# Kernel tuning notes

Hardware: AMD Instinct MI355X
Metric: run time of the kernel (lower is better)

## Reference

```python
import jax, jax.numpy as jnp
import numpy as np

NQ, NS, D, DC, HT = 100000, 2000, 128, 64, 128
B, T = 128, 500
NNZ_HG, NNZ_GCN, NNZ_SIM = 300000, 64000, 1000000
NUM_MV, NUM_QL = 2, 2


def spmm(rows, cols, vals, x, n_rows):
    # y = A @ x, A sparse COO with A[rows[k], cols[k]] = vals[k]
    return jax.ops.segment_sum(vals[:, None] * x[cols], rows, num_segments=n_rows)


def gcn_conv(x, src, dst, W, b, n):
    # PyG-style GCNConv: sym-normalized (A + I), then linear + bias
    h = x @ W
    loop = jnp.arange(n, dtype=src.dtype)
    s = jnp.concatenate([src, loop])
    d = jnp.concatenate([dst, loop])
    deg = jax.ops.segment_sum(jnp.ones(s.shape[0], jnp.float32), d, num_segments=n)
    dinv = jax.lax.rsqrt(jnp.maximum(deg, 1.0))
    norm = dinv[s] * dinv[d]
    return jax.ops.segment_sum(norm[:, None] * h[s], d, num_segments=n) + b


def setup_inputs() -> dict:
    key = jax.random.key(0)
    ks = iter(jax.random.split(key, 64))
    nrm = lambda shape, s=0.05: jax.random.normal(next(ks), shape, jnp.float32) * s
    ri = lambda shape, hi: jax.random.randint(next(ks), shape, 0, hi, jnp.int32)
    inp = {}
    inp['question_seq'] = ri((B, T), NQ)
    inp['skill_seq'] = ri((B, T), NS)
    inp['answer_seq'] = ri((B, T), 2)
    inp['hg_q'] = ri((NNZ_HG,), NQ)
    inp['hg_c'] = ri((NNZ_HG,), NS)
    inp['gcn_src'] = ri((NNZ_GCN,), NS)
    inp['gcn_dst'] = ri((NNZ_GCN,), NS)
    inp['sim_src'] = ri((NNZ_SIM,), NQ)
    inp['sim_dst'] = ri((NNZ_SIM,), NQ)
    inp['hg_vals_qc'] = jax.random.uniform(next(ks), (NNZ_HG,), jnp.float32) * 0.05
    inp['hg_vals_cq'] = jax.random.uniform(next(ks), (NNZ_HG,), jnp.float32) * 0.05
    inp['sim_vals'] = jax.random.uniform(next(ks), (NNZ_SIM,), jnp.float32) * 0.02
    inp['q_emb'] = nrm((NQ + 1, D))
    inp['s_emb'] = nrm((NS + 1, D))
    inp['c_emb'] = nrm((3, DC))
    for nm in ['w_g1', 'w_g2', 'w_g3']:
        inp[nm] = nrm((D, D))
    for nm in ['b_g1', 'b_g2', 'b_g3']:
        inp[nm] = nrm((1, D))
    for i in [1, 2, 3]:
        inp['gcn_w%d' % i] = nrm((D, D))
        inp['gcn_b%d' % i] = nrm((D,))
    for nm in ['w_sg1', 'w_sg2', 'w_qg1', 'w_qg3']:
        inp[nm] = nrm((D, 1))
    for nm in ['b_sg1', 'b_sg2', 'b_qg1', 'b_qg3']:
        inp[nm] = nrm((1,))
    LIN = 2 * D + DC
    inp['w_ih'] = nrm((4 * HT, LIN))
    inp['w_hh'] = nrm((4 * HT, HT))
    inp['b_ih'] = nrm((4 * HT,))
    inp['b_hh'] = nrm((4 * HT,))
    inp['fc1_w'] = nrm((HT + 2 * D, HT))
    inp['fc1_b'] = nrm((HT,))
    inp['fc2_w'] = nrm((HT, 1))
    inp['fc2_b'] = nrm((1,))
    return inp


def reference(question_seq, skill_seq, answer_seq, hg_q, hg_c, gcn_src, gcn_dst,
              sim_src, sim_dst, hg_vals_qc, hg_vals_cq, sim_vals,
              q_emb, s_emb, c_emb, w_g1, w_g2, w_g3, b_g1, b_g2, b_g3,
              gcn_w1, gcn_b1, gcn_w2, gcn_b2, gcn_w3, gcn_b3,
              w_sg1, w_sg2, w_qg1, w_qg3, b_sg1, b_sg2, b_qg1, b_qg3,
              w_ih, w_hh, b_ih, b_hh, fc1_w, fc1_b, fc2_w, fc2_b):
    sig = jax.nn.sigmoid
    # gated (channel-specific) embedding tables, excluding padding row
    one_gate = s_emb[:-1] * sig(s_emb[:-1] @ w_g1 + b_g1)
    two_gate = s_emb[:-1] * sig(s_emb[:-1] @ w_g2 + b_g2)
    three_gate = q_emb[:-1] * sig(q_emb[:-1] @ w_g3 + b_g3)

    # channel 1: multi-view hypergraph conv with residual + mean over layers (dropout p=0 -> identity)
    embs = [one_gate]
    x = one_gate
    for _ in range(NUM_MV):
        m = spmm(hg_q, hg_c, hg_vals_qc, x, NQ)   # HG_qc @ x -> [NQ, D]
        x = spmm(hg_c, hg_q, hg_vals_cq, m, NS)   # HG_cq @ m -> [NS, D]
        x = x + embs[-1]
        embs.append(x)
    one_skill = jnp.mean(jnp.stack(embs), 0)
    one_q = spmm(hg_q, hg_c, hg_vals_qc, one_skill, NQ)  # structural question embs
    one_skill_p = jnp.concatenate([one_skill, s_emb[-1:]], 0)
    one_q_p = jnp.concatenate([one_q, q_emb[-1:]], 0)
    one_b_skill = one_skill_p[skill_seq]   # [B,T,D]
    one_b_q = one_q_p[question_seq]        # [B,T,D]

    # channel 2: 3-layer GCN with relu (dropout p=0)
    x = jax.nn.relu(gcn_conv(two_gate, gcn_src, gcn_dst, gcn_w1, gcn_b1, NS))
    x = jax.nn.relu(gcn_conv(x, gcn_src, gcn_dst, gcn_w2, gcn_b2, NS))
    x = jax.nn.relu(gcn_conv(x, gcn_src, gcn_dst, gcn_w3, gcn_b3, NS))
    two_skill_p = jnp.concatenate([x, s_emb[-1:]], 0)
    two_b_skill = two_skill_p[skill_seq]

    # channel 3: question similarity conv with residual + mean over layers
    embs = [three_gate]
    x = three_gate
    for _ in range(NUM_QL):
        x = spmm(sim_src, sim_dst, sim_vals, x, NQ) + embs[-1]
        embs.append(x)
    three_q = jnp.mean(jnp.stack(embs), 0)
    three_q_p = jnp.concatenate([three_q, q_emb[-1:]], 0)
    three_b_q = three_q_p[question_seq]

    # gated channel fusion
    fused_skill = sig(one_b_skill @ w_sg1 + b_sg1) * one_b_skill \
                + sig(two_b_skill @ w_sg2 + b_sg2) * two_b_skill
    fused_q = sig(one_b_q @ w_qg1 + b_qg1) * one_b_q \
            + sig(three_b_q @ w_qg3 + b_qg3) * three_b_q
    corr = c_emb[answer_seq]  # [B,T,DC]
    lstm_in = jnp.concatenate([fused_q, fused_skill, corr], -1)  # [B,T,2D+DC]

    def step(carry, xt):
        h, c = carry
        z = xt @ w_ih.T + b_ih + h @ w_hh.T + b_hh
        i, f, g, o = jnp.split(z, 4, axis=-1)  # torch LSTM gate order
        c = sig(f) * c + sig(i) * jnp.tanh(g)
        h = sig(o) * jnp.tanh(c)
        return (h, c), h

    b = lstm_in.shape[0]
    h0 = jnp.zeros((b, HT), lstm_in.dtype)
    _, hs = jax.lax.scan(step, (h0, h0), jnp.swapaxes(lstm_in, 0, 1))
    hs = jnp.swapaxes(hs, 0, 1)  # [B,T,HT]

    pred_in = jnp.concatenate([hs, fused_q, fused_skill], -1)  # [B,T,HT+2D]
    preds = sig(jax.nn.relu(pred_in @ fc1_w + fc1_b) @ fc2_w + fc2_b)  # [B,T,1]
    return preds
```

## Files before the change

### kernel.cpp

```cpp
#include <hip/hip_runtime.h>

#define NQc 100000
#define NSc 2000
#define Dc 128
#define DCc 64
#define HTc 128
#define Bc 128
#define Tc 500
#define BTc (Bc*Tc)
#define NNZ_HGc 300000
#define NNZ_GCNc 64000
#define NNZ_SIMc 1000000
#define LINc 320
#define G4c 512

using bf16x8  = __attribute__((ext_vector_type(8))) short;
using floatx4 = __attribute__((ext_vector_type(4))) float;
typedef _Float16 half2v __attribute__((ext_vector_type(2)));

__device__ __forceinline__ float sigf(float x){ return 1.0f/(1.0f + __expf(-x)); }
__device__ __forceinline__ float tanhfast(float x){ return 2.0f*sigf(2.0f*x) - 1.0f; }

__device__ __forceinline__ unsigned short bf16r(float x){
  unsigned u = __float_as_uint(x);
  unsigned r = (u + 0x7FFFu + ((u>>16)&1u)) >> 16;
  return (unsigned short)r;
}
__device__ __forceinline__ unsigned pack2(float2 v){
  return (unsigned)bf16r(v.x) | ((unsigned)bf16r(v.y) << 16);
}
__device__ __forceinline__ float bflo(unsigned u){ return __uint_as_float(u << 16); }
__device__ __forceinline__ float bfhi(unsigned u){ return __uint_as_float(u & 0xFFFF0000u); }

__device__ __forceinline__ float wredsum(float v){
  #pragma unroll
  for (int off=32; off>0; off>>=1) v += __shfl_xor(v, off, 64);
  return v;
}

__global__ void fill_kernel(float* p, float v, int n){
  int i = blockIdx.x*blockDim.x + threadIdx.x;
  if (i<n) p[i] = v;
}

__global__ void cvt_bf16_kernel(const float* __restrict__ in, unsigned short* __restrict__ out, long n){
  long i = (long)blockIdx.x*blockDim.x + threadIdx.x;
  long stride = (long)gridDim.x*blockDim.x;
  for (; i<n; i+=stride) out[i] = bf16r(in[i]);
}

__global__ void cvt_weights_kernel(
    const float* __restrict__ w_ih, unsigned short* __restrict__ w_ih_bf,
    const float* __restrict__ fc1_w, unsigned short* __restrict__ fc1_wT,
    const float* __restrict__ w_g3, unsigned short* __restrict__ w_g3T,
    const float* __restrict__ w_hh, _Float16* __restrict__ w_hh_h,
    const float* __restrict__ b_ih, const float* __restrict__ b_hh, float* __restrict__ biasP)
{
  int i = blockIdx.x*blockDim.x + threadIdx.x;
  const int T0 = G4c*LINc;
  const int T1 = T0 + 384*HTc;
  const int T2 = T1 + Dc*Dc;
  const int T3 = T2 + G4c*HTc;
  const int T4 = T3 + G4c;
  if (i < T0){
    int r = i/LINc, c = i%LINc;
    int rp = (r&127)*4 + (r>>7);
    w_ih_bf[(size_t)rp*LINc + c] = bf16r(w_ih[i]);
  } else if (i < T1){
    int j = i - T0; int r = j/HTc, c = j%HTc;
    fc1_wT[(size_t)c*384 + r] = bf16r(fc1_w[j]);
  } else if (i < T2){
    int j = i - T1; int r = j/Dc, c = j%Dc;
    w_g3T[(size_t)c*Dc + r] = bf16r(w_g3[j]);
  } else if (i < T3){
    int j = i - T2;
    w_hh_h[j] = (_Float16)w_hh[j];
  } else if (i < T4){
    int j = i - T3;
    biasP[(j&127)*4 + (j>>7)] = b_ih[j] + b_hh[j];
  }
}

__global__ void hist_all_kernel(const int* __restrict__ sim_src, int* cnt_sim,
                                const int* __restrict__ hg_q, int* cnt_hgq,
                                const int* __restrict__ hg_c, int* cnt_hgc,
                                const int* __restrict__ gcn_dst, int* cnt_gcn){
  long i = (long)blockIdx.x*blockDim.x + threadIdx.x;
  long stride = (long)gridDim.x*blockDim.x;
  const long T0=NNZ_SIMc, T1=T0+NNZ_HGc, T2=T1+NNZ_HGc, T3=T2+NNZ_GCNc;
  for (; i<T3; i+=stride){
    if (i<T0)      atomicAdd(&cnt_sim[sim_src[i]], 1);
    else if (i<T1) atomicAdd(&cnt_hgq[hg_q[i-T0]], 1);
    else if (i<T2) atomicAdd(&cnt_hgc[hg_c[i-T1]], 1);
    else           atomicAdd(&cnt_gcn[gcn_dst[i-T2]], 1);
  }
}

#define BS_STRIDE 104
__global__ __launch_bounds__(1024) void scan_local_all_kernel(
    const int* __restrict__ cnt_sim, int* rp_sim,
    const int* __restrict__ cnt_hgq, int* rp_hgq,
    const int* __restrict__ cnt_hgc, int* rp_hgc,
    const int* __restrict__ cnt_gcn, int* rp_gcn,
    int* __restrict__ bsum, float* __restrict__ dinv)
{
  __shared__ int buf[1024];
  int b = blockIdx.x, tid = threadIdx.x;
  const int* cnt; int* rp; int* bs; int n; int lb; int seg;
  if (b < 98)      { seg=0; cnt=cnt_sim; rp=rp_sim; n=NQc; lb=b; }
  else if (b <196) { seg=1; cnt=cnt_hgq; rp=rp_hgq; n=NQc; lb=b-98; }
  else if (b <198) { seg=2; cnt=cnt_hgc; rp=rp_hgc; n=NSc; lb=b-196; }
  else             { seg=3; cnt=cnt_gcn; rp=rp_gcn; n=NSc; lb=b-198; }
  bs = bsum + seg*BS_STRIDE;
  int i = lb*1024 + tid;
  int v = (i<n) ? cnt[i] : 0;
  if (seg==3 && i<n) dinv[i] = rsqrtf((float)v + 1.0f);
  buf[tid] = v;
  __syncthreads();
  for (int off=1; off<1024; off<<=1){
    int t = (tid>=off) ? buf[tid-off] : 0;
    __syncthreads();
    buf[tid] += t;
    __syncthreads();
  }
  if (i<n) rp[i] = buf[tid] - v;
  if (tid==1023) bs[lb] = buf[1023];
}
__global__ __launch_bounds__(128) void scan_bsum_all_kernel(int* bsum){
  __shared__ int s[128];
  int seg = blockIdx.x, tid = threadIdx.x;
  int nb = (seg<2) ? 98 : 2;
  int* bs = bsum + seg*BS_STRIDE;
  int v = (tid<nb) ? bs[tid] : 0;
  s[tid] = v;
  __syncthreads();
  for (int off=1; off<128; off<<=1){
    int t = (tid>=off) ? s[tid-off] : 0;
    __syncthreads();
    s[tid] += t;
    __syncthreads();
  }
  if (tid<nb) bs[tid] = s[tid] - v;
  if (tid==0) bs[nb] = s[127];
}
__global__ void scan_add_all_kernel(
    int* rp_sim, int* cnt_sim, int* rp_hgq, int* cnt_hgq,
    int* rp_hgc, int* cnt_hgc, int* rp_gcn, int* cnt_gcn,
    const int* __restrict__ bsum)
{
  int b = blockIdx.x, tid = threadIdx.x;
  int* rp; int* cur; const int* bs; int n; int lb; int nb;
  if (b < 391)      { rp=rp_sim; cur=cnt_sim; bs=bsum;               n=NQc; lb=b;     nb=98; }
  else if (b < 782) { rp=rp_hgq; cur=cnt_hgq; bs=bsum+BS_STRIDE;     n=NQc; lb=b-391; nb=98; }
  else if (b < 790) { rp=rp_hgc; cur=cnt_hgc; bs=bsum+2*BS_STRIDE;   n=NSc; lb=b-782; nb=2; }
  else              { rp=rp_gcn; cur=cnt_gcn; bs=bsum+3*BS_STRIDE;   n=NSc; lb=b-790; nb=2; }
  int i = lb*256 + tid;
  if (i<n){ int r = rp[i] + bs[i>>10]; rp[i]=r; cur[i]=r; }
  if (lb==0 && tid==0) rp[n] = bs[nb];
}

__global__ void scatter_all_kernel(
    const int* __restrict__ sim_src, const int* __restrict__ sim_dst, const float* __restrict__ sim_vals,
    int* cur_sim, int* col_sim, float* val_sim,
    const int* __restrict__ hg_q, const int* __restrict__ hg_c,
    const float* __restrict__ hg_vals_qc, const float* __restrict__ hg_vals_cq,
    int* cur_hgq, int* col_hgq, float* val_hgq,
    int* cur_hgc, int* col_hgc, float* val_hgc,
    const int* __restrict__ gcn_dst, const int* __restrict__ gcn_src,
    int* cur_gcn, int* src_gcn)
{
  long i = (long)blockIdx.x*blockDim.x + threadIdx.x;
  long stride = (long)gridDim.x*blockDim.x;
  const long T0=NNZ_SIMc, T1=T0+NNZ_HGc, T2=T1+NNZ_HGc, T3=T2+NNZ_GCNc;
  for (; i<T3; i+=stride){
    if (i<T0){
      int r = sim_src[i]; int p = atomicAdd(&cur_sim[r],1);
      col_sim[p] = sim_dst[i]; val_sim[p] = sim_vals[i];
    } else if (i<T1){
      long j=i-T0; int r = hg_q[j]; int p = atomicAdd(&cur_hgq[r],1);
      col_hgq[p] = hg_c[j]; val_hgq[p] = hg_vals_qc[j];
    } else if (i<T2){
      long j=i-T1; int r = hg_c[j]; int p = atomicAdd(&cur_hgc[r],1);
      col_hgc[p] = hg_q[j]; val_hgc[p] = hg_vals_cq[j];
    } else {
      long j=i-T2; int r = gcn_dst[j]; int p = atomicAdd(&cur_gcn[r],1);
      src_gcn[p] = gcn_src[j];
    }
  }
}

#define BM 64
#define BN 64
#define BK 16
__global__ __launch_bounds__(256) void gemm_kernel(
    const float* __restrict__ A, int lda,
    const float* __restrict__ Bm, float* __restrict__ C,
    unsigned short* __restrict__ Cbf, float* __restrict__ Ccopy,
    const float* __restrict__ bias, const float* __restrict__ gsrc,
    int M, int N, int K, int ep)
{
  __shared__ float As[BM][BK+4];
  __shared__ float Bs[BK][BN+4];
  int tid = threadIdx.x;
  int tx = tid & 15, ty = tid >> 4;
  int mBase = blockIdx.y*BM, nBase = blockIdx.x*BN;
  float acc[4][4];
  #pragma unroll
  for (int i=0;i<4;i++)
    #pragma unroll
    for (int j=0;j<4;j++) acc[i][j]=0.f;
  int arow = tid>>2, ac4 = tid&3;
  for (int kt=0; kt<K; kt+=BK){
    {
      int m = mBase + arow;
      float4 v = make_float4(0.f,0.f,0.f,0.f);
      if (m < M) v = *(const float4*)(A + (size_t)m*lda + kt + ac4*4);
      *(float4*)&As[arow][ac4*4] = v;
    }
    {
      int kr = tid>>4, c4 = tid&15;
      float4 v = *(const float4*)(Bm + (size_t)(kt+kr)*N + nBase + c4*4);
      *(float4*)&Bs[kr][c4*4] = v;
    }
    __syncthreads();
    #pragma unroll
    for (int k=0;k<BK;k++){
      float a0=As[ty*4+0][k],a1=As[ty*4+1][k],a2=As[ty*4+2][k],a3=As[ty*4+3][k];
      float b0=Bs[k][tx*4+0],b1=Bs[k][tx*4+1],b2=Bs[k][tx*4+2],b3=Bs[k][tx*4+3];
      acc[0][0]+=a0*b0; acc[0][1]+=a0*b1; acc[0][2]+=a0*b2; acc[0][3]+=a0*b3;
      acc[1][0]+=a1*b0; acc[1][1]+=a1*b1; acc[1][2]+=a1*b2; acc[1][3]+=a1*b3;
      acc[2][0]+=a2*b0; acc[2][1]+=a2*b1; acc[2][2]+=a2*b2; acc[2][3]+=a2*b3;
      acc[3][0]+=a3*b0; acc[3][1]+=a3*b1; acc[3][2]+=a3*b2; acc[3][3]+=a3*b3;
    }
    __syncthreads();
  }
  #pragma unroll
  for (int i=0;i<4;i++){
    int m = mBase + ty*4 + i;
    if (m >= M) continue;
    #pragma unroll
    for (int j=0;j<4;j++){
      int n = nBase + tx*4 + j;
      float v = acc[i][j];
      if (bias)  v += bias[n];
      if (ep==1)      v = gsrc[(size_t)m*N + n] * sigf(v);
      C[(size_t)m*N + n] = v;
      if (Cbf)   Cbf[(size_t)m*N + n] = bf16r(v);
      if (Ccopy) Ccopy[(size_t)m*N + n] = v;
    }
  }
}

__global__ __launch_bounds__(256) void mfma_gemm_kernel(
    const unsigned short* __restrict__ A1, int lda1,
    const unsigned short* __restrict__ A2, int lda2, int ksplit,
    const unsigned short* __restrict__ Bt,
    float* __restrict__ C, unsigned short* __restrict__ Cbf,
    const float* __restrict__ bias, const float* __restrict__ bias2,
    const float* __restrict__ gsrc,
    const float* __restrict__ fc2w, const float* __restrict__ fc2b, float* __restrict__ outp,
    int M, int N, int K, int ep)
{
  __shared__ unsigned short Asm[128*64];
  __shared__ unsigned short Bsm[128*64];
  __shared__ float rps[2][128];
  int tid = threadIdx.x;
  int wave = tid>>6, lane = tid&63;
  int quad = lane>>4, l16 = lane&15;
  int m0 = blockIdx.y*128, n0 = blockIdx.x*128;
  int wm = (wave&1)*64, wn = (wave>>1)*64;
  floatx4 acc[4][4];
  #pragma unroll
  for (int i=0;i<4;i++)
    #pragma unroll
    for (int j=0;j<4;j++) acc[i][j] = (floatx4){0.f,0.f,0.f,0.f};

  for (int kt=0; kt<K; kt+=64){
    #pragma unroll
    for (int i=0;i<4;i++){
      int idx = i*256 + tid;
      int row = idx>>3, blk = idx&7;
      int kcol = kt + blk*8;
      {
        const unsigned short* src = (kcol < ksplit)
            ? (A1 + (size_t)(m0+row)*lda1 + kcol)
            : (A2 + (size_t)(m0+row)*lda2 + (kcol - ksplit));
        float4 v = *(const float4*)src;
        *(float4*)&Asm[row*64 + ((blk ^ (row&7))<<3)] = v;
      }
      {
        const unsigned short* src = Bt + (size_t)(n0+row)*K + kcol;
        float4 v = *(const float4*)src;
        *(float4*)&Bsm[row*64 + ((blk ^ (row&7))<<3)] = v;
      }
    }
    __syncthreads();
    #pragma unroll
    for (int ks=0; ks<2; ks++){
      bf16x8 af[4], bfr[4];
      #pragma unroll
      for (int mt=0;mt<4;mt++){
        int row = wm + mt*16 + l16;
        int blk = ks*4 + quad;
        af[mt] = *(const bf16x8*)&Asm[row*64 + ((blk ^ (row&7))<<3)];
      }
      #pragma unroll
      for (int nt=0;nt<4;nt++){
        int row = wn + nt*16 + l16;
        int blk = ks*4 + quad;
        bfr[nt] = *(const bf16x8*)&Bsm[row*64 + ((blk ^ (row&7))<<3)];
      }
      #pragma unroll
      for (int mt=0;mt<4;mt++)
        #pragma unroll
        for (int nt=0;nt<4;nt++)
          acc[mt][nt] = __builtin_amdgcn_mfma_f32_16x16x32_bf16(af[mt], bfr[nt], acc[mt][nt], 0,0,0);
    }
    __syncthreads();
  }
  if (ep == 3){
    float fw[4], fb[4];
    #pragma unroll
    for (int nt=0;nt<4;nt++){ int col = wn + nt*16 + l16; fw[nt] = fc2w[col]; fb[nt] = bias[col]; }
    #pragma unroll
    for (int mt=0;mt<4;mt++){
      #pragma unroll
      for (int r=0;r<4;r++){
        float s = 0.f;
        #pragma unroll
        for (int nt=0;nt<4;nt++){
          float v = acc[mt][nt][r] + fb[nt];
          v = fmaxf(v, 0.f);
          s += v*fw[nt];
        }
        s += __shfl_xor(s,1); s += __shfl_xor(s,2); s += __shfl_xor(s,4); s += __shfl_xor(s,8);
        if (l16 == 0) rps[wave>>1][wm + mt*16 + quad*4 + r] = s;
      }
    }
    __syncthreads();
    if (tid < 128){
      int row = m0 + tid;
      if (row < M) outp[row] = sigf(rps[0][tid] + rps[1][tid] + fc2b[0]);
    }
    return;
  }
  #pragma unroll
  for (int mt=0;mt<4;mt++){
    #pragma unroll
    for (int nt=0;nt<4;nt++){
      int col = n0 + wn + nt*16 + l16;
      #pragma unroll
      for (int r=0;r<4;r++){
        int row = m0 + wm + mt*16 + quad*4 + r;
        if (row < M){
          float v = acc[mt][nt][r];
          if (bias)  v += bias[col];
          if (bias2) v += bias2[col];
          if (ep==1)      v = gsrc[(size_t)row*N + col] * sigf(v);
          else if (ep==2) v = fmaxf(v, 0.f);
          C[(size_t)row*N + col] = v;
          if (Cbf) Cbf[(size_t)row*N + col] = bf16r(v);
        }
      }
    }
  }
}

__global__ __launch_bounds__(256) void spmm_bf_kernel(
    const int* __restrict__ rowptr, const int* __restrict__ col, const float* __restrict__ val,
    const unsigned short* __restrict__ xbf, const float* __restrict__ resid,
    const float* __restrict__ resid2, float beta,
    float* __restrict__ y, unsigned short* __restrict__ ybf,
    float* __restrict__ sumbuf, unsigned short* __restrict__ sumbf,
    float alpha, int nrows)
{
  int w = (int)((blockIdx.x*(unsigned)blockDim.x + threadIdx.x) >> 6);
  int lane = threadIdx.x & 63;
  if (w >= nrows) return;
  int beg = rowptr[w], end = rowptr[w+1];
  const unsigned* x2 = (const unsigned*)xbf;
  float ax=0.f, ay=0.f;
  int k = beg;
  for (; k+4 <= end; k+=4){
    int c0=col[k], c1=col[k+1], c2=col[k+2], c3=col[k+3];
    float v0=val[k], v1=val[k+1], v2=val[k+2], v3=val[k+3];
    unsigned u0 = x2[(size_t)c0*64 + lane];
    unsigned u1 = x2[(size_t)c1*64 + lane];
    unsigned u2 = x2[(size_t)c2*64 + lane];
    unsigned u3 = x2[(size_t)c3*64 + lane];
    ax += v0*bflo(u0); ay += v0*bfhi(u0);
    ax += v1*bflo(u1); ay += v1*bfhi(u1);
    ax += v2*bflo(u2); ay += v2*bfhi(u2);
    ax += v3*bflo(u3); ay += v3*bfhi(u3);
  }
  for (; k<end; k++){
    int c = col[k]; float v = val[k];
    unsigned u = x2[(size_t)c*64 + lane];
    ax += v*bflo(u); ay += v*bfhi(u);
  }
  ax*=alpha; ay*=alpha;
  if (resid){ float2 r = ((const float2*)resid)[(size_t)w*64+lane]; ax+=r.x; ay+=r.y; }
  if (resid2){ float2 r = ((const float2*)resid2)[(size_t)w*64+lane]; ax+=beta*r.x; ay+=beta*r.y; }
  float2 o; o.x=ax; o.y=ay;
  ((float2*)y)[(size_t)w*64+lane] = o;
  if (ybf) ((unsigned*)ybf)[(size_t)w*64+lane] = pack2(o);
  if (sumbuf){
    float2 s = ((float2*)sumbuf)[(size_t)w*64+lane];
    s.x+=ax; s.y+=ay;
    ((float2*)sumbuf)[(size_t)w*64+lane] = s;
    if (sumbf) ((unsigned*)sumbf)[(size_t)w*64+lane] = pack2(s);
  }
}

__global__ __launch_bounds__(256) void gcn_spmm_kernel(
    const int* __restrict__ rowptr, const int* __restrict__ src, const float* __restrict__ dinv,
    const float* __restrict__ h, const float* __restrict__ bias, float* __restrict__ out, int nrows)
{
  int w = (int)((blockIdx.x*(unsigned)blockDim.x + threadIdx.x) >> 6);
  int lane = threadIdx.x & 63;
  if (w >= nrows) return;
  int beg = rowptr[w], end = rowptr[w+1];
  const float2* h2 = (const float2*)h;
  float dr = dinv[w];
  float2 self = h2[(size_t)w*64+lane];
  float ax = dr*self.x, ay = dr*self.y;
  int k = beg;
  for (; k+4 <= end; k+=4){
    int s0=src[k], s1=src[k+1], s2=src[k+2], s3=src[k+3];
    float d0=dinv[s0], d1=dinv[s1], d2=dinv[s2], d3=dinv[s3];
    float2 h0=h2[(size_t)s0*64+lane], h1v=h2[(size_t)s1*64+lane];
    float2 h2v=h2[(size_t)s2*64+lane], h3=h2[(size_t)s3*64+lane];
    ax += d0*h0.x + d1*h1v.x + d2*h2v.x + d3*h3.x;
    ay += d0*h0.y + d1*h1v.y + d2*h2v.y + d3*h3.y;
  }
  for (; k<end; k++){
    int s = src[k]; float ds = dinv[s];
    float2 hv = h2[(size_t)s*64+lane];
    ax += ds*hv.x; ay += ds*hv.y;
  }
  ax*=dr; ay*=dr;
  float2 b2 = ((const float2*)bias)[lane];
  float2 o; o.x = fmaxf(ax + b2.x, 0.f); o.y = fmaxf(ay + b2.y, 0.f);
  ((float2*)out)[(size_t)w*64+lane] = o;
}

__global__ __launch_bounds__(256) void gather_fuse_kernel(
    const int* __restrict__ q_seq, const int* __restrict__ s_seq, const int* __restrict__ a_seq,
    const float* __restrict__ skill_sum, const float* __restrict__ one_q,
    const float* __restrict__ two_skill, const float* __restrict__ three_sum,
    const float* __restrict__ s_emb, const float* __restrict__ q_emb, const float* __restrict__ c_emb,
    const float* __restrict__ w_sg1, const float* __restrict__ w_sg2,
    const float* __restrict__ w_qg1, const float* __restrict__ w_qg3,
    const float* __restrict__ b_sg1, const float* __restrict__ b_sg2,
    const float* __restrict__ b_qg1, const float* __restrict__ b_qg3,
    unsigned short* __restrict__ lstm_in_bf)
{
  int idx = (int)((blockIdx.x*(unsigned)blockDim.x + threadIdx.x) >> 6);
  int lane = threadIdx.x & 63;
  if (idx >= BTc) return;
  int q = q_seq[idx], s = s_seq[idx], a = a_seq[idx];
  float2 obs, tbs, obq, tbq;
  if (s < NSc){
    obs = ((const float2*)(skill_sum + (size_t)s*Dc))[lane];
    obs.x *= (1.f/3.f); obs.y *= (1.f/3.f);
    tbs = ((const float2*)(two_skill + (size_t)s*Dc))[lane];
  } else {
    obs = ((const float2*)(s_emb + (size_t)NSc*Dc))[lane];
    tbs = obs;
  }
  if (q < NQc){
    obq = ((const float2*)(one_q + (size_t)q*Dc))[lane];
    tbq = ((const float2*)(three_sum + (size_t)q*Dc))[lane];
    tbq.x *= (1.f/3.f); tbq.y *= (1.f/3.f);
  } else {
    obq = ((const float2*)(q_emb + (size_t)NQc*Dc))[lane];
    tbq = obq;
  }
  float2 w1 = ((const float2*)w_sg1)[lane];
  float2 w2 = ((const float2*)w_sg2)[lane];
  float2 w3 = ((const float2*)w_qg1)[lane];
  float2 w4 = ((const float2*)w_qg3)[lane];
  float p1 = wredsum(obs.x*w1.x + obs.y*w1.y);
  float p2 = wredsum(tbs.x*w2.x + tbs.y*w2.y);
  float p3 = wredsum(obq.x*w3.x + obq.y*w3.y);
  float p4 = wredsum(tbq.x*w4.x + tbq.y*w4.y);
  float g1 = sigf(p1 + b_sg1[0]);
  float g2 = sigf(p2 + b_sg2[0]);
  float g3 = sigf(p3 + b_qg1[0]);
  float g4 = sigf(p4 + b_qg3[0]);
  float2 fs, fq;
  fs.x = g1*obs.x + g2*tbs.x; fs.y = g1*obs.y + g2*tbs.y;
  fq.x = g3*obq.x + g4*tbq.x; fq.y = g3*obq.y + g4*tbq.y;
  unsigned* rowb = (unsigned*)(lstm_in_bf + (size_t)idx*LINc);
  rowb[lane]      = pack2(fq);
  rowb[64 + lane] = pack2(fs);
  if (lane < 32){
    float2 cv = ((const float2*)(c_emb + (size_t)a*DCc))[lane];
    rowb[128 + lane] = pack2(cv);
  }
}

__global__ __launch_bounds__(512, 2) void lstm_kernel(
    const float* __restrict__ xpart, const _Float16* __restrict__ w_hh_h,
    unsigned short* __restrict__ hs_bf)
{
  __shared__ __align__(16) _Float16 h_lds[2][HTc];
  int b = blockIdx.x, tid = threadIdx.x;
  int j = tid >> 2, sub = tid & 3;
  unsigned wbits[4][16];
  #pragma unroll
  for (int g=0; g<4; g++){
    const unsigned* wp = (const unsigned*)(w_hh_h + (size_t)(g*128 + j)*HTc + sub*32);
    #pragma unroll
    for (int i=0;i<16;i++) wbits[g][i] = wp[i];
  }
  #pragma unroll
  for (int g=0; g<4; g++)
    #pragma unroll
    for (int i=0;i<16;i++)
      asm volatile("" : "+v"(wbits[g][i]));
  if (tid < HTc) h_lds[0][tid] = (_Float16)0.f;
  float c = 0.f;
  __syncthreads();
  const float* xp = xpart + (size_t)b*Tc*G4c;
  unsigned short* hb = hs_bf + (size_t)b*Tc*HTc;
  float xcur = xp[tid];
  for (int t=0; t<Tc; t++){
    int tn = (t+1 < Tc) ? t+1 : Tc-1;
    float xnext = xp[(size_t)tn*G4c + tid];
    int cur = t & 1;
    float4 hv[4];
    const float4* hsrc = (const float4*)&h_lds[cur][sub*32];
    #pragma unroll
    for (int i=0;i<4;i++) hv[i] = hsrc[i];
    const half2v* hh = (const half2v*)hv;
    float p0=0.f,p1=0.f,p2=0.f,p3=0.f;
    #pragma unroll
    for (int i=0;i<16;i++){
      half2v h2 = hh[i];
#if __has_builtin(__builtin_amdgcn_fdot2)
      p0 = __builtin_amdgcn_fdot2(__builtin_bit_cast(half2v, wbits[0][i]), h2, p0, false);
      p1 = __builtin_amdgcn_fdot2(__builtin_bit_cast(half2v, wbits[1][i]), h2, p1, false);
      p2 = __builtin_amdgcn_fdot2(__builtin_bit_cast(half2v, wbits[2][i]), h2, p2, false);
      p3 = __builtin_amdgcn_fdot2(__builtin_bit_cast(half2v, wbits[3][i]), h2, p3, false);
#else
      half2v w0 = __builtin_bit_cast(half2v, wbits[0][i]);
      half2v w1 = __builtin_bit_cast(half2v, wbits[1][i]);
      half2v w2 = __builtin_bit_cast(half2v, wbits[2][i]);
      half2v w3 = __builtin_bit_cast(half2v, wbits[3][i]);
      p0 += (float)w0.x*(float)h2.x + (float)w0.y*(float)h2.y;
      p1 += (float)w1.x*(float)h2.x + (float)w1.y*(float)h2.y;
      p2 += (float)w2.x*(float)h2.x + (float)w2.y*(float)h2.y;
      p3 += (float)w3.x*(float)h2.x + (float)w3.y*(float)h2.y;
#endif
    }
    if (sub==0) p0 += xcur; else if (sub==1) p1 += xcur; else if (sub==2) p2 += xcur; else p3 += xcur;
    p0 += __shfl_xor(p0,1); p0 += __shfl_xor(p0,2);
    p1 += __shfl_xor(p1,1); p1 += __shfl_xor(p1,2);
    p2 += __shfl_xor(p2,1); p2 += __shfl_xor(p2,2);
    p3 += __shfl_xor(p3,1); p3 += __shfl_xor(p3,2);
    float ig=sigf(p0), fg=sigf(p1), gg=tanhfast(p2), og=sigf(p3);
    c = fg*c + ig*gg;
    float h = og*tanhfast(c);
    if (sub == 0){
      h_lds[1-cur][j] = (_Float16)h;
      hb[(size_t)t*HTc + j] = bf16r(h);
    }
    __syncthreads();
    xcur = xnext;
  }
}

extern "C" void kernel_launch(void* const* d_in, const int* in_sizes, int n_in,
                              void* d_out, int out_size, void* d_ws, size_t ws_size,
                              hipStream_t stream)
{
  const int* question_seq=(const int*)d_in[0];
  const int* skill_seq   =(const int*)d_in[1];
  const int* answer_seq  =(const int*)d_in[2];
  const int* hg_q        =(const int*)d_in[3];
  const int* hg_c        =(const int*)d_in[4];
  const int* gcn_src     =(const int*)d_in[5];
  const int* gcn_dst     =(const int*)d_in[6];
  const int* sim_src     =(const int*)d_in[7];
  const int* sim_dst     =(const int*)d_in[8];
  const float* hg_vals_qc=(const float*)d_in[9];
  const float* hg_vals_cq=(const float*)d_in[10];
  const float* sim_vals  =(const float*)d_in[11];
  const float* q_emb     =(const float*)d_in[12];
  const float* s_emb     =(const float*)d_in[13];
  const float* c_emb     =(const float*)d_in[14];
  const float* w_g1=(const float*)d_in[15];
  const float* w_g2=(const float*)d_in[16];
  const float* w_g3=(const float*)d_in[17];
  const float* b_g1=(const float*)d_in[18];
  const float* b_g2=(const float*)d_in[19];
  const float* b_g3=(const float*)d_in[20];
  const float* gcn_w1=(const float*)d_in[21];
  const float* gcn_b1=(const float*)d_in[22];
  const float* gcn_w2=(const float*)d_in[23];
  const float* gcn_b2=(const float*)d_in[24];
  const float* gcn_w3=(const float*)d_in[25];
  const float* gcn_b3=(const float*)d_in[26];
  const float* w_sg1=(const float*)d_in[27];
  const float* w_sg2=(const float*)d_in[28];
  const float* w_qg1=(const float*)d_in[29];
  const float* w_qg3=(const float*)d_in[30];
  const float* b_sg1=(const float*)d_in[31];
  const float* b_sg2=(const float*)d_in[32];
  const float* b_qg1=(const float*)d_in[33];
  const float* b_qg3=(const float*)d_in[34];
  const float* w_ih=(const float*)d_in[35];
  const float* w_hh=(const float*)d_in[36];
  const float* b_ih=(const float*)d_in[37];
  const float* b_hh=(const float*)d_in[38];
  const float* fc1_w=(const float*)d_in[39];
  const float* fc1_b=(const float*)d_in[40];
  const float* fc2_w=(const float*)d_in[41];
  const float* fc2_b=(const float*)d_in[42];
  (void)in_sizes; (void)n_in;
  float* outp = (float*)d_out;

  char* base = (char*)d_ws;
  size_t off = 0;
  auto alloc = [&](size_t bytes)->size_t{ size_t r = off; off = (off + bytes + 255) & ~(size_t)255; return r; };

  size_t XPbytes = (size_t)BTc*G4c*4;
  size_t o_XP     = alloc(XPbytes);
  size_t o_libf   = alloc((size_t)BTc*LINc*2);
  size_t o_hsbf   = alloc((size_t)BTc*HTc*2);
  size_t o_qembbf = alloc((size_t)100096*Dc*2);
  size_t o_bfY    = alloc((size_t)NQc*Dc*2);
  size_t o_wihbf  = alloc((size_t)G4c*LINc*2);
  size_t o_fc1wT  = alloc((size_t)HTc*384*2);
  size_t o_wg3T   = alloc((size_t)Dc*Dc*2);
  size_t o_whhh   = alloc((size_t)G4c*HTc*2);
  size_t o_biasP  = alloc((size_t)G4c*4);
  if (off > ws_size){
    fill_kernel<<<(out_size+255)/256, 256, 0, stream>>>(outp, -1.0f, out_size);
    return;
  }

  char* xp = base + o_XP;
  size_t poff = 0;
  auto pall = [&](size_t bytes)->size_t{ size_t r = poff; poff = (poff + bytes + 255) & ~(size_t)255; return r; };
  size_t p_A       = pall((size_t)NQc*Dc*4);
  size_t p_B       = pall((size_t)NQc*Dc*4);
  size_t p_col_sim = pall((size_t)NNZ_SIMc*4);
  size_t p_val_sim = pall((size_t)NNZ_SIMc*4);
  size_t p_col_hgq = pall((size_t)NNZ_HGc*4);
  size_t p_val_hgq = pall((size_t)NNZ_HGc*4);
  size_t p_col_hgc = pall((size_t)NNZ_HGc*4);
  size_t p_val_hgc = pall((size_t)NNZ_HGc*4);
  size_t p_src_gcn = pall((size_t)NNZ_GCNc*4);
  size_t p_rp_sim  = pall((size_t)(NQc+1)*4);
  size_t p_rp_hgq  = pall((size_t)(NQc+1)*4);
  size_t p_rp_hgc  = pall((size_t)(NSc+1)*4);
  size_t p_rp_gcn  = pall((size_t)(NSc+1)*4);
  size_t p_cnt_sim = pall((size_t)NQc*4);
  size_t p_cnt_hgq = pall((size_t)NQc*4);
  size_t p_cnt_hgc = pall((size_t)NSc*4);
  size_t p_cnt_gcn = pall((size_t)NSc*4);
  size_t p_cnt_end = poff;
  size_t p_bsum    = pall((size_t)4*BS_STRIDE*4);
  size_t p_dinv    = pall((size_t)NSc*4);
  size_t p_onegate = pall((size_t)NSc*Dc*4);
  size_t p_twogate = pall((size_t)NSc*Dc*4);
  size_t p_ssum    = pall((size_t)NSc*Dc*4);
  size_t p_sxA     = pall((size_t)NSc*Dc*4);
  size_t p_sxB     = pall((size_t)NSc*Dc*4);
  size_t p_gxA     = pall((size_t)NSc*Dc*4);
  size_t p_gxB     = pall((size_t)NSc*Dc*4);
  size_t p_htmp    = pall((size_t)NSc*Dc*4);
  size_t p_ogbf    = pall((size_t)NSc*Dc*2);
  size_t p_sxBbf   = pall((size_t)NSc*Dc*2);
  size_t p_ssumbf  = pall((size_t)NSc*Dc*2);
  if (poff > XPbytes){
    fill_kernel<<<(out_size+255)/256, 256, 0, stream>>>(outp, -2.0f, out_size);
    return;
  }

  float* Abuf    = (float*)(xp + p_A);
  float* Bbuf    = (float*)(xp + p_B);
  int*   col_sim = (int*)(xp + p_col_sim);
  float* val_sim = (float*)(xp + p_val_sim);
  int*   col_hgq = (int*)(xp + p_col_hgq);
  float* val_hgq = (float*)(xp + p_val_hgq);
  int*   col_hgc = (int*)(xp + p_col_hgc);
  float* val_hgc = (float*)(xp + p_val_hgc);
  int*   src_gcn = (int*)(xp + p_src_gcn);
  int*   rp_sim  = (int*)(xp + p_rp_sim);
  int*   rp_hgq  = (int*)(xp + p_rp_hgq);
  int*   rp_hgc  = (int*)(xp + p_rp_hgc);
  int*   rp_gcn  = (int*)(xp + p_rp_gcn);
  int*   cnt_sim = (int*)(xp + p_cnt_sim);
  int*   cnt_hgq = (int*)(xp + p_cnt_hgq);
  int*   cnt_hgc = (int*)(xp + p_cnt_hgc);
  int*   cnt_gcn = (int*)(xp + p_cnt_gcn);
  int*   bsum    = (int*)(xp + p_bsum);
  float* dinv    = (float*)(xp + p_dinv);
  float* one_gate= (float*)(xp + p_onegate);
  float* two_gate= (float*)(xp + p_twogate);
  float* ssum    = (float*)(xp + p_ssum);
  float* sxA     = (float*)(xp + p_sxA);
  float* sxB     = (float*)(xp + p_sxB);
  float* gxA     = (float*)(xp + p_gxA);
  float* gxB     = (float*)(xp + p_gxB);
  float* htmp    = (float*)(xp + p_htmp);
  unsigned short* og_bf   = (unsigned short*)(xp + p_ogbf);
  unsigned short* sxB_bf  = (unsigned short*)(xp + p_sxBbf);
  unsigned short* ssum_bf = (unsigned short*)(xp + p_ssumbf);

  float* xpart   = (float*)xp;
  unsigned short* lstm_in_bf = (unsigned short*)(base + o_libf);
  unsigned short* hs_bf      = (unsigned short*)(base + o_hsbf);
  unsigned short* q_emb_bf   = (unsigned short*)(base + o_qembbf);
  unsigned short* bfX        = (unsigned short*)(base + o_qembbf);
  unsigned short* bfY        = (unsigned short*)(base + o_bfY);
  unsigned short* w_ih_bf    = (unsigned short*)(base + o_wihbf);
  unsigned short* fc1_wT     = (unsigned short*)(base + o_fc1wT);
  unsigned short* w_g3T      = (unsigned short*)(base + o_wg3T);
  _Float16*       w_hh_h     = (_Float16*)(base + o_whhh);
  float*          biasP      = (float*)(base + o_biasP);

  auto gemm32 = [&](const float* A, int lda, const float* Bp, float* Cp,
                    unsigned short* Cbf, float* Ccopy, const float* bias,
                    const float* gsrc, int M, int N, int K, int ep){
    dim3 g(N/64, (M+63)/64), b(256);
    gemm_kernel<<<g, b, 0, stream>>>(A, lda, Bp, Cp, Cbf, Ccopy, bias, gsrc, M, N, K, ep);
  };
  auto spmm = [&](const int* rp, const int* col, const float* val, const unsigned short* xb,
                  const float* resid, const float* resid2, float beta,
                  float* y, unsigned short* yb, float* sum, unsigned short* sumbf,
                  float alpha, int nrows){
    spmm_bf_kernel<<<(nrows+3)/4, 256, 0, stream>>>(rp, col, val, xb, resid, resid2, beta, y, yb, sum, sumbf, alpha, nrows);
  };

  hipMemsetAsync(xp + p_cnt_sim, 0, p_cnt_end - p_cnt_sim, stream);
  hist_all_kernel<<<2048, 256, 0, stream>>>(sim_src, cnt_sim, hg_q, cnt_hgq, hg_c, cnt_hgc, gcn_dst, cnt_gcn);
  scan_local_all_kernel<<<200, 1024, 0, stream>>>(cnt_sim, rp_sim, cnt_hgq, rp_hgq,
                                                  cnt_hgc, rp_hgc, cnt_gcn, rp_gcn, bsum, dinv);
  scan_bsum_all_kernel<<<4, 128, 0, stream>>>(bsum);
  scan_add_all_kernel<<<798, 256, 0, stream>>>(rp_sim, cnt_sim, rp_hgq, cnt_hgq,
                                               rp_hgc, cnt_hgc, rp_gcn, cnt_gcn, bsum);
  scatter_all_kernel<<<2048, 256, 0, stream>>>(
      sim_src, sim_dst, sim_vals, cnt_sim, col_sim, val_sim,
      hg_q, hg_c, hg_vals_qc, hg_vals_cq,
      cnt_hgq, col_hgq, val_hgq, cnt_hgc, col_hgc, val_hgc,
      gcn_dst, gcn_src, cnt_gcn, src_gcn);

  cvt_bf16_kernel<<<2048, 256, 0, stream>>>(q_emb, q_emb_bf, (long)(NQc+1)*Dc);
  cvt_weights_kernel<<<1154, 256, 0, stream>>>(w_ih, w_ih_bf, fc1_w, fc1_wT, w_g3, w_g3T,
                                               w_hh, w_hh_h, b_ih, b_hh, biasP);

  {
    dim3 g(1, (NQc+127)/128);
    mfma_gemm_kernel<<<g, 256, 0, stream>>>(q_emb_bf, Dc, q_emb_bf, Dc, Dc, w_g3T,
                                            Abuf, bfY, b_g3, nullptr, q_emb,
                                            nullptr, nullptr, nullptr, NQc, Dc, Dc, 1);
  }
  spmm(rp_sim, col_sim, val_sim, bfY, Abuf, nullptr, 0.f, Bbuf, bfX,    nullptr, nullptr, 1.f, NQc);
  spmm(rp_sim, col_sim, val_sim, bfX, Abuf, Bbuf, 2.f,   Abuf, nullptr, nullptr, nullptr, 1.f, NQc);

  gemm32(s_emb, Dc, w_g1, one_gate, og_bf, ssum, b_g1, s_emb, NSc, Dc, Dc, 1);
  gemm32(s_emb, Dc, w_g2, two_gate, nullptr, nullptr, b_g2, s_emb, NSc, Dc, Dc, 1);

  spmm(rp_hgq, col_hgq, val_hgq, og_bf,  nullptr,  nullptr, 0.f, Bbuf, bfY,    nullptr, nullptr, 1.f, NQc);
  spmm(rp_hgc, col_hgc, val_hgc, bfY,    one_gate, nullptr, 0.f, sxB,  sxB_bf, ssum,    nullptr, 1.f, NSc);
  spmm(rp_hgq, col_hgq, val_hgq, sxB_bf, nullptr,  nullptr, 0.f, Bbuf, bfY,    nullptr, nullptr, 1.f, NQc);
  spmm(rp_hgc, col_hgc, val_hgc, bfY,    sxB,      nullptr, 0.f, sxA,  nullptr, ssum,   ssum_bf, 1.f, NSc);
  spmm(rp_hgq, col_hgq, val_hgq, ssum_bf, nullptr, nullptr, 0.f, Bbuf, nullptr, nullptr, nullptr, 1.f/3.f, NQc);

  gemm32(two_gate, Dc, gcn_w1, htmp, nullptr, nullptr, nullptr, nullptr, NSc, Dc, Dc, 0);
  gcn_spmm_kernel<<<(NSc+3)/4, 256, 0, stream>>>(rp_gcn, src_gcn, dinv, htmp, gcn_b1, gxA, NSc);
  gemm32(gxA, Dc, gcn_w2, htmp, nullptr, nullptr, nullptr, nullptr, NSc, Dc, Dc, 0);
  gcn_spmm_kernel<<<(NSc+3)/4, 256, 0, stream>>>(rp_gcn, src_gcn, dinv, htmp, gcn_b2, gxB, NSc);
  gemm32(gxB, Dc, gcn_w3, htmp, nullptr, nullptr, nullptr, nullptr, NSc, Dc, Dc, 0);
  gcn_spmm_kernel<<<(NSc+3)/4, 256, 0, stream>>>(rp_gcn, src_gcn, dinv, htmp, gcn_b3, gxA, NSc);

  gather_fuse_kernel<<<(BTc+3)/4, 256, 0, stream>>>(
      question_seq, skill_seq, answer_seq,
      ssum, Bbuf, gxA, Abuf,
      s_emb, q_emb, c_emb,
      w_sg1, w_sg2, w_qg1, w_qg3, b_sg1, b_sg2, b_qg1, b_qg3,
      lstm_in_bf);

  {
    dim3 g(G4c/128, BTc/128);
    mfma_gemm_kernel<<<g, 256, 0, stream>>>(lstm_in_bf, LINc, lstm_in_bf, LINc, LINc, w_ih_bf,
                                            xpart, nullptr, biasP, nullptr, nullptr,
                                            nullptr, nullptr, nullptr, BTc, G4c, LINc, 0);
  }

  lstm_kernel<<<Bc, 512, 0, stream>>>(xpart, w_hh_h, hs_bf);

  {
    dim3 g(1, BTc/128);
    mfma_gemm_kernel<<<g, 256, 0, stream>>>(hs_bf, HTc, lstm_in_bf, LINc, HTc, fc1_wT,
                                            nullptr, nullptr, fc1_b, nullptr, nullptr,
                                            fc2_w, fc2_b, outp, BTc, 128, 384, 3);
  }
}
```

Baseline: 1.407 ms.

## Store large NQ-sized intermediates in bf16 instead of fp32

Replaces the fp32 100000x128 intermediate buffers (residuals and SpMM outputs on question nodes) with bf16 buffers, so SpMM residual reads and output writes, and the gather in the fuse kernel, move half the bytes. It skips fp32 stores where only the bf16 copy is consumed and drops the asm register pinning of LSTM weights in favor of plain half2 arrays. The cost is lower precision for the residual chain and the gathered question embeddings, and a possible change in register allocation for the LSTM.

```diff
diff --git a/kernel.cpp b/kernel.cpp
--- a/kernel.cpp
+++ b/kernel.cpp
@@ -358,7 +358,7 @@
           if (bias2) v += bias2[col];
           if (ep==1)      v = gsrc[(size_t)row*N + col] * sigf(v);
           else if (ep==2) v = fmaxf(v, 0.f);
-          C[(size_t)row*N + col] = v;
+          if (C)   C[(size_t)row*N + col] = v;
           if (Cbf) Cbf[(size_t)row*N + col] = bf16r(v);
         }
       }
@@ -368,8 +368,10 @@
 
 __global__ __launch_bounds__(256) void spmm_bf_kernel(
     const int* __restrict__ rowptr, const int* __restrict__ col, const float* __restrict__ val,
-    const unsigned short* __restrict__ xbf, const float* __restrict__ resid,
-    const float* __restrict__ resid2, float beta,
+    const unsigned short* __restrict__ xbf,
+    const float* __restrict__ residF,
+    const unsigned short* __restrict__ residB,
+    const unsigned short* __restrict__ residB2, float beta,
     float* __restrict__ y, unsigned short* __restrict__ ybf,
     float* __restrict__ sumbuf, unsigned short* __restrict__ sumbf,
     float alpha, int nrows)
@@ -399,10 +401,11 @@
     ax += v*bflo(u); ay += v*bfhi(u);
   }
   ax*=alpha; ay*=alpha;
-  if (resid){ float2 r = ((const float2*)resid)[(size_t)w*64+lane]; ax+=r.x; ay+=r.y; }
-  if (resid2){ float2 r = ((const float2*)resid2)[(size_t)w*64+lane]; ax+=beta*r.x; ay+=beta*r.y; }
+  if (residF){ float2 r = ((const float2*)residF)[(size_t)w*64+lane]; ax+=r.x; ay+=r.y; }
+  if (residB){ unsigned u = ((const unsigned*)residB)[(size_t)w*64+lane]; ax+=bflo(u); ay+=bfhi(u); }
+  if (residB2){ unsigned u = ((const unsigned*)residB2)[(size_t)w*64+lane]; ax+=beta*bflo(u); ay+=beta*bfhi(u); }
   float2 o; o.x=ax; o.y=ay;
-  ((float2*)y)[(size_t)w*64+lane] = o;
+  if (y)   ((float2*)y)[(size_t)w*64+lane] = o;
   if (ybf) ((unsigned*)ybf)[(size_t)w*64+lane] = pack2(o);
   if (sumbuf){
     float2 s = ((float2*)sumbuf)[(size_t)w*64+lane];
@@ -446,8 +449,8 @@
 
 __global__ __launch_bounds__(256) void gather_fuse_kernel(
     const int* __restrict__ q_seq, const int* __restrict__ s_seq, const int* __restrict__ a_seq,
-    const float* __restrict__ skill_sum, const float* __restrict__ one_q,
-    const float* __restrict__ two_skill, const float* __restrict__ three_sum,
+    const float* __restrict__ skill_sum, const unsigned short* __restrict__ one_q_bf,
+    const float* __restrict__ two_skill, const unsigned short* __restrict__ three_sum_bf,
     const float* __restrict__ s_emb, const float* __restrict__ q_emb, const float* __restrict__ c_emb,
     const float* __restrict__ w_sg1, const float* __restrict__ w_sg2,
     const float* __restrict__ w_qg1, const float* __restrict__ w_qg3,
@@ -469,9 +472,10 @@
     tbs = obs;
   }
   if (q < NQc){
-    obq = ((const float2*)(one_q + (size_t)q*Dc))[lane];
-    tbq = ((const float2*)(three_sum + (size_t)q*Dc))[lane];
-    tbq.x *= (1.f/3.f); tbq.y *= (1.f/3.f);
+    unsigned u1 = ((const unsigned*)(one_q_bf + (size_t)q*Dc))[lane];
+    obq.x = bflo(u1); obq.y = bfhi(u1);
+    unsigned u2 = ((const unsigned*)(three_sum_bf + (size_t)q*Dc))[lane];
+    tbq.x = bflo(u2)*(1.f/3.f); tbq.y = bfhi(u2)*(1.f/3.f);
   } else {
     obq = ((const float2*)(q_emb + (size_t)NQc*Dc))[lane];
     tbq = obq;
@@ -507,18 +511,13 @@
   __shared__ __align__(16) _Float16 h_lds[2][HTc];
   int b = blockIdx.x, tid = threadIdx.x;
   int j = tid >> 2, sub = tid & 3;
-  unsigned wbits[4][16];
+  half2v w[4][16];
   #pragma unroll
   for (int g=0; g<4; g++){
-    const unsigned* wp = (const unsigned*)(w_hh_h + (size_t)(g*128 + j)*HTc + sub*32);
-    #pragma unroll
-    for (int i=0;i<16;i++) wbits[g][i] = wp[i];
-  }
-  #pragma unroll
-  for (int g=0; g<4; g++)
-    #pragma unroll
-    for (int i=0;i<16;i++)
-      asm volatile("" : "+v"(wbits[g][i]));
+    const half2v* wp = (const half2v*)(w_hh_h + (size_t)(g*128 + j)*HTc + sub*32);
+    #pragma unroll
+    for (int i=0;i<16;i++) w[g][i] = wp[i];
+  }
   if (tid < HTc) h_lds[0][tid] = (_Float16)0.f;
   float c = 0.f;
   __syncthreads();
@@ -539,19 +538,15 @@
     for (int i=0;i<16;i++){
       half2v h2 = hh[i];
 #if __has_builtin(__builtin_amdgcn_fdot2)
-      p0 = __builtin_amdgcn_fdot2(__builtin_bit_cast(half2v, wbits[0][i]), h2, p0, false);
-      p1 = __builtin_amdgcn_fdot2(__builtin_bit_cast(half2v, wbits[1][i]), h2, p1, false);
-      p2 = __builtin_amdgcn_fdot2(__builtin_bit_cast(half2v, wbits[2][i]), h2, p2, false);
-      p3 = __builtin_amdgcn_fdot2(__builtin_bit_cast(half2v, wbits[3][i]), h2, p3, false);
+      p0 = __builtin_amdgcn_fdot2(w[0][i], h2, p0, false);
+      p1 = __builtin_amdgcn_fdot2(w[1][i], h2, p1, false);
+      p2 = __builtin_amdgcn_fdot2(w[2][i], h2, p2, false);
+      p3 = __builtin_amdgcn_fdot2(w[3][i], h2, p3, false);
 #else
-      half2v w0 = __builtin_bit_cast(half2v, wbits[0][i]);
-      half2v w1 = __builtin_bit_cast(half2v, wbits[1][i]);
-      half2v w2 = __builtin_bit_cast(half2v, wbits[2][i]);
-      half2v w3 = __builtin_bit_cast(half2v, wbits[3][i]);
-      p0 += (float)w0.x*(float)h2.x + (float)w0.y*(float)h2.y;
-      p1 += (float)w1.x*(float)h2.x + (float)w1.y*(float)h2.y;
-      p2 += (float)w2.x*(float)h2.x + (float)w2.y*(float)h2.y;
-      p3 += (float)w3.x*(float)h2.x + (float)w3.y*(float)h2.y;
+      p0 += (float)w[0][i].x*(float)h2.x + (float)w[0][i].y*(float)h2.y;
+      p1 += (float)w[1][i].x*(float)h2.x + (float)w[1][i].y*(float)h2.y;
+      p2 += (float)w[2][i].x*(float)h2.x + (float)w[2][i].y*(float)h2.y;
+      p3 += (float)w[3][i].x*(float)h2.x + (float)w[3][i].y*(float)h2.y;
 #endif
     }
     if (sub==0) p0 += xcur; else if (sub==1) p1 += xcur; else if (sub==2) p2 += xcur; else p3 += xcur;
@@ -630,7 +625,6 @@
   size_t o_libf   = alloc((size_t)BTc*LINc*2);
   size_t o_hsbf   = alloc((size_t)BTc*HTc*2);
   size_t o_qembbf = alloc((size_t)100096*Dc*2);
-  size_t o_bfY    = alloc((size_t)NQc*Dc*2);
   size_t o_wihbf  = alloc((size_t)G4c*LINc*2);
   size_t o_fc1wT  = alloc((size_t)HTc*384*2);
   size_t o_wg3T   = alloc((size_t)Dc*Dc*2);
@@ -644,8 +638,9 @@
   char* xp = base + o_XP;
   size_t poff = 0;
   auto pall = [&](size_t bytes)->size_t{ size_t r = poff; poff = (poff + bytes + 255) & ~(size_t)255; return r; };
-  size_t p_A       = pall((size_t)NQc*Dc*4);
-  size_t p_B       = pall((size_t)NQc*Dc*4);
+  size_t p_bfY     = pall((size_t)NQc*Dc*2);
+  size_t p_bfX     = pall((size_t)NQc*Dc*2);
+  size_t p_bfZ     = pall((size_t)NQc*Dc*2);
   size_t p_col_sim = pall((size_t)NNZ_SIMc*4);
   size_t p_val_sim = pall((size_t)NNZ_SIMc*4);
   size_t p_col_hgq = pall((size_t)NNZ_HGc*4);
@@ -680,8 +675,9 @@
     return;
   }
 
-  float* Abuf    = (float*)(xp + p_A);
-  float* Bbuf    = (float*)(xp + p_B);
+  unsigned short* bfY = (unsigned short*)(xp + p_bfY);
+  unsigned short* bfX = (unsigned short*)(xp + p_bfX);
+  unsigned short* bfZ = (unsigned short*)(xp + p_bfZ);
   int*   col_sim = (int*)(xp + p_col_sim);
   float* val_sim = (float*)(xp + p_val_sim);
   int*   col_hgq = (int*)(xp + p_col_hgq);
@@ -715,8 +711,6 @@
   unsigned short* lstm_in_bf = (unsigned short*)(base + o_libf);
   unsigned short* hs_bf      = (unsigned short*)(base + o_hsbf);
   unsigned short* q_emb_bf   = (unsigned short*)(base + o_qembbf);
-  unsigned short* bfX        = (unsigned short*)(base + o_qembbf);
-  unsigned short* bfY        = (unsigned short*)(base + o_bfY);
   unsigned short* w_ih_bf    = (unsigned short*)(base + o_wihbf);
   unsigned short* fc1_wT     = (unsigned short*)(base + o_fc1wT);
   unsigned short* w_g3T      = (unsigned short*)(base + o_wg3T);
@@ -730,10 +724,12 @@
     gemm_kernel<<<g, b, 0, stream>>>(A, lda, Bp, Cp, Cbf, Ccopy, bias, gsrc, M, N, K, ep);
   };
   auto spmm = [&](const int* rp, const int* col, const float* val, const unsigned short* xb,
-                  const float* resid, const float* resid2, float beta,
+                  const float* residF, const unsigned short* residB,
+                  const unsigned short* residB2, float beta,
                   float* y, unsigned short* yb, float* sum, unsigned short* sumbf,
                   float alpha, int nrows){
-    spmm_bf_kernel<<<(nrows+3)/4, 256, 0, stream>>>(rp, col, val, xb, resid, resid2, beta, y, yb, sum, sumbf, alpha, nrows);
+    spmm_bf_kernel<<<(nrows+3)/4, 256, 0, stream>>>(rp, col, val, xb, residF, residB, residB2, beta,
+                                                    y, yb, sum, sumbf, alpha, nrows);
   };
 
   hipMemsetAsync(xp + p_cnt_sim, 0, p_cnt_end - p_cnt_sim, stream);
@@ -756,20 +752,27 @@
   {
     dim3 g(1, (NQc+127)/128);
     mfma_gemm_kernel<<<g, 256, 0, stream>>>(q_emb_bf, Dc, q_emb_bf, Dc, Dc, w_g3T,
-                                            Abuf, bfY, b_g3, nullptr, q_emb,
+                                            nullptr, bfY, b_g3, nullptr, q_emb,
                                             nullptr, nullptr, nullptr, NQc, Dc, Dc, 1);
   }
-  spmm(rp_sim, col_sim, val_sim, bfY, Abuf, nullptr, 0.f, Bbuf, bfX,    nullptr, nullptr, 1.f, NQc);
-  spmm(rp_sim, col_sim, val_sim, bfX, Abuf, Bbuf, 2.f,   Abuf, nullptr, nullptr, nullptr, 1.f, NQc);
+  spmm(rp_sim, col_sim, val_sim, bfY, nullptr, bfY, nullptr, 0.f,
+       nullptr, bfX, nullptr, nullptr, 1.f, NQc);
+  spmm(rp_sim, col_sim, val_sim, bfX, nullptr, bfY, bfX, 2.f,
+       nullptr, bfZ, nullptr, nullptr, 1.f, NQc);
 
   gemm32(s_emb, Dc, w_g1, one_gate, og_bf, ssum, b_g1, s_emb, NSc, Dc, Dc, 1);
   gemm32(s_emb, Dc, w_g2, two_gate, nullptr, nullptr, b_g2, s_emb, NSc, Dc, Dc, 1);
 
-  spmm(rp_hgq, col_hgq, val_hgq, og_bf,  nullptr,  nullptr, 0.f, Bbuf, bfY,    nullptr, nullptr, 1.f, NQc);
-  spmm(rp_hgc, col_hgc, val_hgc, bfY,    one_gate, nullptr, 0.f, sxB,  sxB_bf, ssum,    nullptr, 1.f, NSc);
-  spmm(rp_hgq, col_hgq, val_hgq, sxB_bf, nullptr,  nullptr, 0.f, Bbuf, bfY,    nullptr, nullptr, 1.f, NQc);
-  spmm(rp_hgc, col_hgc, val_hgc, bfY,    sxB,      nullptr, 0.f, sxA,  nullptr, ssum,   ssum_bf, 1.f, NSc);
-  spmm(rp_hgq, col_hgq, val_hgq, ssum_bf, nullptr, nullptr, 0.f, Bbuf, nullptr, nullptr, nullptr, 1.f/3.f, NQc);
+  spmm(rp_hgq, col_hgq, val_hgq, og_bf,  nullptr, nullptr, nullptr, 0.f,
+       nullptr, bfY, nullptr, nullptr, 1.f, NQc);
+  spmm(rp_hgc, col_hgc, val_hgc, bfY,    one_gate, nullptr, nullptr, 0.f,
+       sxB, sxB_bf, ssum, nullptr, 1.f, NSc);
+  spmm(rp_hgq, col_hgq, val_hgq, sxB_bf, nullptr, nullptr, nullptr, 0.f,
+       nullptr, bfY, nullptr, nullptr, 1.f, NQc);
+  spmm(rp_hgc, col_hgc, val_hgc, bfY,    sxB, nullptr, nullptr, 0.f,
+       nullptr, nullptr, ssum, ssum_bf, 1.f, NSc);
+  spmm(rp_hgq, col_hgq, val_hgq, ssum_bf, nullptr, nullptr, nullptr, 0.f,
+       nullptr, bfX, nullptr, nullptr, 1.f/3.f, NQc);
 
   gemm32(two_gate, Dc, gcn_w1, htmp, nullptr, nullptr, nullptr, nullptr, NSc, Dc, Dc, 0);
   gcn_spmm_kernel<<<(NSc+3)/4, 256, 0, stream>>>(rp_gcn, src_gcn, dinv, htmp, gcn_b1, gxA, NSc);
@@ -780,7 +783,7 @@
 
   gather_fuse_kernel<<<(BTc+3)/4, 256, 0, stream>>>(
       question_seq, skill_seq, answer_seq,
-      ssum, Bbuf, gxA, Abuf,
+      ssum, bfX, gxA, bfZ,
       s_emb, q_emb, c_emb,
       w_sg1, w_sg2, w_qg1, w_qg3, b_sg1, b_sg2, b_qg1, b_qg3,
       lstm_in_bf);
```

New measurement: 1.390 ms. Within noise of the previous version (-1.2%).
